# Kernel tuning notes

Measured on AMD Instinct MI355X. Metric: run time of the kernel, lower is better.

Reference implementation:

```python
import jax, jax.numpy as jnp
import numpy as np

EPS = 1e-3  # matches torch module eps
NUM_FEATURES = 64


def setup_inputs() -> dict:
    key = jax.random.key(0)
    X = jax.random.normal(key, (128, NUM_FEATURES, 56, 56), dtype=jnp.float32)
    return {"X": X}


def reference(X):
    # Training-mode decorrelated batch norm (ZCA whitening via eigendecomposition).
    N, C = X.shape[0], X.shape[1]
    # [N, C, H, W] -> [C, N*H*W]
    x = jnp.reshape(jnp.swapaxes(X, 0, 1), (C, -1))
    m = x.shape[1]
    mean = jnp.mean(x, axis=-1, keepdims=True)
    xc = x - mean
    # sigma = eps*I + (1/m) * xc @ xc^T   (C x C, SPD)
    sigma = EPS * jnp.eye(C, dtype=X.dtype) + (xc @ xc.T) / m
    # SVD of an SPD matrix == eigendecomposition; use symmetric eigh.
    eig, u = jnp.linalg.eigh(sigma)
    # wm = u @ diag(eig^-1/2) @ u^T  (inverse matrix square root)
    wm = (u * jax.lax.rsqrt(eig)) @ u.T
    xn = wm @ xc  # whiten
    # [C, N*H*W] -> [N, C, H, W]
    Xn = jnp.swapaxes(jnp.reshape(xn, (C, N) + X.shape[2:]), 0, 1)
    return Xn
```

## Files before the change

kernel.cpp:

```cpp
#include <hip/hip_runtime.h>
#include <stdint.h>

#define CCH   64
#define HWSZ  3136
#define NB    128
#define MCOLS 401408
#define TK    128
#define NTILES 3136
#define LDK   136
#define LDB   72
#define SLOT  4160
#define WS_TAIL 16512
#define RG    16
#define K1MAX 512
#define LDT   72
#define K3NB  1024
#define K3T   6272

typedef short bf16x8 __attribute__((ext_vector_type(8)));
typedef float f32x4  __attribute__((ext_vector_type(4)));
typedef unsigned short u16x4 __attribute__((ext_vector_type(4)));

__device__ __forceinline__ unsigned short f2bf(float f) {
    union { float f; uint32_t u; } v; v.f = f;
    uint32_t r = v.u + 0x7fffu + ((v.u >> 16) & 1u);
    return (unsigned short)(r >> 16);
}
__device__ __forceinline__ float bf2f(unsigned short h) {
    union { uint32_t u; float f; } v; v.u = ((uint32_t)h) << 16; return v.f;
}
__device__ __forceinline__ uint32_t fbits(float f) {
    union { float f; uint32_t u; } v; v.f = f; return v.u;
}
__device__ __forceinline__ float bcast(uint32_t u) {
    union { uint32_t u; float f; } v; v.u = u; return v.f;
}

__global__ __launch_bounds__(256) void k1_gram(const float* __restrict__ X,
                                               float* __restrict__ part,
                                               int nb) {
    __shared__ __align__(16) unsigned short tile[CCH * LDK];
    const int tid = threadIdx.x;
    const int w = tid >> 6, l = tid & 63;

    f32x4 acc[4];
    #pragma unroll
    for (int b = 0; b < 4; ++b) acc[b] = (f32x4){0.f, 0.f, 0.f, 0.f};
    float sacc[16];
    #pragma unroll
    for (int i = 0; i < 16; ++i) sacc[i] = 0.f;

    float2 xv[16];

    uint32_t t = blockIdx.x;
    {
        const uint32_t s = t * TK + 2u * (uint32_t)l;
        const uint32_t n = s / HWSZ;
        const uint32_t hw = s - n * HWSZ;
        const size_t base = (size_t)n * (CCH * HWSZ) + hw + (size_t)w * HWSZ;
        #pragma unroll
        for (int i = 0; i < 16; ++i)
            xv[i] = *(const float2*)(X + base + (size_t)i * (4u * HWSZ));
    }

    for (;;) {
        __syncthreads();
        #pragma unroll
        for (int i = 0; i < 16; ++i) {
            sacc[i] += xv[i].x + xv[i].y;
            const int c = 4 * i + w;
            *(uint32_t*)&tile[c * LDK + 2 * l] =
                (uint32_t)f2bf(xv[i].x) | ((uint32_t)f2bf(xv[i].y) << 16);
        }
        __syncthreads();

        const uint32_t tn = t + (uint32_t)nb;
        const bool more = tn < NTILES;
        if (more) {
            const uint32_t s = tn * TK + 2u * (uint32_t)l;
            const uint32_t n = s / HWSZ;
            const uint32_t hw = s - n * HWSZ;
            const size_t base = (size_t)n * (CCH * HWSZ) + hw + (size_t)w * HWSZ;
            #pragma unroll
            for (int i = 0; i < 16; ++i)
                xv[i] = *(const float2*)(X + base + (size_t)i * (4u * HWSZ));
        }

        #pragma unroll
        for (int k0 = 0; k0 < TK; k0 += 32) {
            const int koff = k0 + ((l >> 4) << 3);
            const bf16x8 fa = *(const bf16x8*)&tile[(16 * w + (l & 15)) * LDK + koff];
            #pragma unroll
            for (int bj = 0; bj < 4; ++bj) {
                const bf16x8 fb = *(const bf16x8*)&tile[(16 * bj + (l & 15)) * LDK + koff];
                acc[bj] = __builtin_amdgcn_mfma_f32_16x16x32_bf16(fa, fb, acc[bj], 0, 0, 0);
            }
        }

        if (!more) break;
        t = tn;
    }

    float* pg = part + (size_t)blockIdx.x * SLOT;
    #pragma unroll
    for (int bj = 0; bj < 4; ++bj) {
        #pragma unroll
        for (int r = 0; r < 4; ++r) {
            const int row = 16 * w + ((l >> 4) << 2) + r;
            const int col = 16 * bj + (l & 15);
            pg[row * 64 + col] = acc[bj][r];
        }
    }
    #pragma unroll
    for (int i = 0; i < 16; ++i) {
        float v = sacc[i];
        #pragma unroll
        for (int m = 32; m > 0; m >>= 1) v += __shfl_xor(v, m, 64);
        if (l == 0) pg[4096 + 4 * i + w] = v;
    }
}

__global__ __launch_bounds__(256) void k1b1_reduce(const float* __restrict__ part,
                                                   float* __restrict__ part2,
                                                   int nb) {
    const int bx = blockIdx.x;
    const int g = bx / 17;
    const int e = (bx - g * 17) * 256 + threadIdx.x;
    if (e >= SLOT) return;
    float a0 = 0.f, a1 = 0.f, a2 = 0.f, a3 = 0.f;
    int b = g;
    for (; b + 3 * RG < nb; b += 4 * RG) {
        a0 += part[(size_t)b * SLOT + e];
        a1 += part[(size_t)(b + RG) * SLOT + e];
        a2 += part[(size_t)(b + 2 * RG) * SLOT + e];
        a3 += part[(size_t)(b + 3 * RG) * SLOT + e];
    }
    for (; b < nb; b += RG) a0 += part[(size_t)b * SLOT + e];
    part2[(size_t)g * SLOT + e] = (a0 + a1) + (a2 + a3);
}

__device__ __forceinline__ bf16x8 ldfrag_h(const unsigned short* H, int rowbase, int k0, int l) {
    const int row = rowbase + (l & 15);
    const int koff = k0 + ((l >> 4) << 3);
    return *(const bf16x8*)&H[row * LDB + koff];
}
__device__ __forceinline__ bf16x8 ldfrag_lo(const float* F, bf16x8 hi, int rowbase, int k0, int l) {
    const int row = rowbase + (l & 15);
    const int koff = k0 + ((l >> 4) << 3);
    const float* p = F + row * 64 + koff;
    bf16x8 lo;
    #pragma unroll
    for (int j = 0; j < 8; ++j)
        lo[j] = (short)f2bf(p[j] - bf2f((unsigned short)hi[j]));
    return lo;
}

__device__ void mm_plain(const unsigned short* Lh, const unsigned short* Rh,
                         unsigned short* DH, float* DF, int tid) {
    const int w = tid >> 6, l = tid & 63;
    f32x4 acc[4];
    #pragma unroll
    for (int b = 0; b < 4; ++b) acc[b] = (f32x4){0.f, 0.f, 0.f, 0.f};
    #pragma unroll
    for (int k0 = 0; k0 < 64; k0 += 32) {
        const bf16x8 la = ldfrag_h(Lh, 16 * w, k0, l);
        #pragma unroll
        for (int b = 0; b < 4; ++b) {
            const bf16x8 rb = ldfrag_h(Rh, 16 * b, k0, l);
            acc[b] = __builtin_amdgcn_mfma_f32_16x16x32_bf16(la, rb, acc[b], 0, 0, 0);
        }
    }
    __syncthreads();
    #pragma unroll
    for (int b = 0; b < 4; ++b) {
        #pragma unroll
        for (int r = 0; r < 4; ++r) {
            const int row = 16 * w + ((l >> 4) << 2) + r;
            const int col = 16 * b + (l & 15);
            const float v = acc[b][r];
            if (DH) DH[row * LDB + col] = f2bf(v);
            if (DF) DF[row * 64 + col] = v;
        }
    }
    __syncthreads();
}

__device__ void mm_split(const unsigned short* Lh, const float* Lf,
                         const unsigned short* Rh, const float* Rf,
                         unsigned short* DH, float* DF, int tid) {
    const int w = tid >> 6, l = tid & 63;
    f32x4 acc[4];
    #pragma unroll
    for (int b = 0; b < 4; ++b) acc[b] = (f32x4){0.f, 0.f, 0.f, 0.f};
    #pragma unroll
    for (int k0 = 0; k0 < 64; k0 += 32) {
        const bf16x8 lah = ldfrag_h(Lh, 16 * w, k0, l);
        const bf16x8 lal = ldfrag_lo(Lf, lah, 16 * w, k0, l);
        #pragma unroll
        for (int b = 0; b < 4; ++b) {
            const bf16x8 rbh = ldfrag_h(Rh, 16 * b, k0, l);
            const bf16x8 rbl = ldfrag_lo(Rf, rbh, 16 * b, k0, l);
            acc[b] = __builtin_amdgcn_mfma_f32_16x16x32_bf16(lah, rbh, acc[b], 0, 0, 0);
            acc[b] = __builtin_amdgcn_mfma_f32_16x16x32_bf16(lah, rbl, acc[b], 0, 0, 0);
            acc[b] = __builtin_amdgcn_mfma_f32_16x16x32_bf16(lal, rbh, acc[b], 0, 0, 0);
        }
    }
    __syncthreads();
    #pragma unroll
    for (int b = 0; b < 4; ++b) {
        #pragma unroll
        for (int r = 0; r < 4; ++r) {
            const int row = 16 * w + ((l >> 4) << 2) + r;
            const int col = 16 * b + (l & 15);
            const float v = acc[b][r];
            if (DH) DH[row * LDB + col] = f2bf(v);
            if (DF) DF[row * 64 + col] = v;
        }
    }
    __syncthreads();
}

__global__ __launch_bounds__(256) void k2_ns(const float* __restrict__ part2,
                                             float* __restrict__ ws) {
    float* bvec = ws + 8256;
    float* Ag = ws + 8320;
    unsigned short* wmh = (unsigned short*)(ws + 12416);
    unsigned short* wml = (unsigned short*)(ws + 14464);

    __shared__ float Zf[4096];
    __shared__ float Sf[4096];
    __shared__ __align__(16) unsigned short Ah[64 * LDB];
    __shared__ __align__(16) unsigned short ZhA[64 * LDB];
    __shared__ __align__(16) unsigned short Bh[64 * LDB];
    __shared__ float mu[64];
    __shared__ float sred[1];

    const int tid = threadIdx.x;
    const float invm = 1.0f / (float)MCOLS;

    if (tid < 64) {
        float a = 0.f;
        #pragma unroll
        for (int b = 0; b < RG; ++b) a += part2[(size_t)b * SLOT + 4096 + tid];
        mu[tid] = a * invm;
    }
    __syncthreads();

    #pragma unroll
    for (int j = 0; j < 16; ++j) {
        const int e = tid * 16 + j;
        const int i = e >> 6, c = e & 63;
        float a0 = 0.f, a1 = 0.f, a2 = 0.f, a3 = 0.f;
        #pragma unroll
        for (int b = 0; b < RG; b += 4) {
            a0 += part2[(size_t)(b + 0) * SLOT + e];
            a1 += part2[(size_t)(b + 1) * SLOT + e];
            a2 += part2[(size_t)(b + 2) * SLOT + e];
            a3 += part2[(size_t)(b + 3) * SLOT + e];
        }
        const float g = (a0 + a1) + (a2 + a3);
        Sf[e] = g * invm - mu[i] * mu[c] + ((i == c) ? 1e-3f : 0.0f);
    }
    __syncthreads();

    if (tid < 64) {
        float rs = 0.f;
        #pragma unroll
        for (int j = 0; j < 64; ++j) {
            const int c = (j + tid) & 63;
            rs += fabsf(Sf[tid * 64 + c]);
        }
        #pragma unroll
        for (int m = 32; m > 0; m >>= 1) rs = fmaxf(rs, __shfl_xor(rs, m, 64));
        if (tid == 0) sred[0] = rs;
    }
    __syncthreads();
    const float s = sred[0];
    const float invs = 1.0f / s;

    #pragma unroll
    for (int j = 0; j < 16; ++j) {
        const int e = tid * 16 + j;
        const int i = e >> 6, c = e & 63;
        const float a = Sf[e] * invs;
        Ag[e] = a;
        Ah[i * LDB + c] = f2bf(a);
        const float z = (i == c) ? 1.0f : 0.0f;
        Zf[e] = z;
        ZhA[i * LDB + c] = f2bf(z);
    }
    __syncthreads();

    for (int itn = 0; itn < 4; ++itn) {
        mm_plain(ZhA, ZhA, Bh, nullptr, tid);
        mm_plain(Ah, Bh, Bh, nullptr, tid);
        mm_plain(ZhA, Bh, nullptr, Sf, tid);
        #pragma unroll
        for (int j = 0; j < 16; ++j) {
            const int e = tid * 16 + j;
            const int i = e >> 6, c = e & 63;
            const float z = 1.5f * Zf[e] - 0.5f * Sf[e];
            Zf[e] = z;
            ZhA[i * LDB + c] = f2bf(z);
        }
        __syncthreads();
    }

    mm_split(ZhA, Zf, ZhA, Zf, Bh, Sf, tid);
    mm_split(Ah, Ag, Bh, Sf, Bh, Sf, tid);
    mm_split(ZhA, Zf, Bh, Sf, nullptr, Sf, tid);

    const float wsq = 1.0f / sqrtf(s);
    #pragma unroll
    for (int j = 0; j < 16; ++j) {
        const int e = tid * 16 + j;
        const float z = 1.5f * Zf[e] - 0.5f * Sf[e];
        Zf[e] = z;
        const float wv = z * wsq;
        const unsigned short h = f2bf(wv);
        wmh[e] = h;
        wml[e] = f2bf(wv - bf2f(h));
    }
    __syncthreads();

    if (tid < 64) {
        float acc = 0.f;
        #pragma unroll
        for (int j = 0; j < 64; ++j) {
            const int c = (j + tid) & 63;
            acc += Zf[tid * 64 + c] * mu[c];
        }
        bvec[tid] = acc * wsq;
    }
}

__global__ __launch_bounds__(256) void k3_whiten(const float* __restrict__ X,
                                                 const float* __restrict__ ws,
                                                 float* __restrict__ out) {
    __shared__ __align__(16) unsigned short xh[64 * LDT];
    __shared__ __align__(16) unsigned short xl[64 * LDT];
    const int tid = threadIdx.x;
    const int w = tid >> 6, l = tid & 63;
    const int lm = l & 15;
    const int koffL = (l >> 4) << 3;

    const unsigned short* __restrict__ wmh = (const unsigned short*)(ws + 12416);
    const unsigned short* __restrict__ wml = (const unsigned short*)(ws + 14464);
    const float* __restrict__ bvec = ws + 8256;

    bf16x8 fbh[2][4], fbl[2][4];
    #pragma unroll
    for (int kk = 0; kk < 2; ++kk) {
        #pragma unroll
        for (int cb = 0; cb < 4; ++cb) {
            const int c = cb * 16 + lm;
            fbh[kk][cb] = *(const bf16x8*)&wmh[c * 64 + kk * 32 + koffL];
            fbl[kk][cb] = *(const bf16x8*)&wml[c * 64 + kk * 32 + koffL];
        }
    }
    float bv[4];
    #pragma unroll
    for (int cb = 0; cb < 4; ++cb) bv[cb] = bvec[cb * 16 + lm];

    float xv[16];
    uint32_t g = blockIdx.x;
    size_t base;
    {
        const uint32_t n = g / 49u;
        const uint32_t hw0 = (g - n * 49u) * 64u;
        base = (size_t)n * (CCH * HWSZ) + hw0;
        #pragma unroll
        for (int u = 0; u < 16; ++u)
            xv[u] = X[base + (size_t)(w * 16 + u) * HWSZ + l];
    }

    const int frow = (16 * w + lm) * LDT;
    const int p0 = 16 * w + ((l >> 4) << 2);

    for (;;) {
        __syncthreads();
        #pragma unroll
        for (int uu = 0; uu < 4; ++uu) {
            const int j0 = uu * 4;
            const uint32_t a0 = fbits(xv[j0 + 0]);
            const uint32_t a1 = fbits(xv[j0 + 1]);
            const uint32_t a2 = fbits(xv[j0 + 2]);
            const uint32_t a3 = fbits(xv[j0 + 3]);
            uint2 hv, lv;
            hv.x = __builtin_amdgcn_perm(a1, a0, 0x07060302u);
            hv.y = __builtin_amdgcn_perm(a3, a2, 0x07060302u);
            const float r0 = xv[j0 + 0] - bcast(a0 & 0xFFFF0000u);
            const float r1 = xv[j0 + 1] - bcast(a1 & 0xFFFF0000u);
            const float r2 = xv[j0 + 2] - bcast(a2 & 0xFFFF0000u);
            const float r3 = xv[j0 + 3] - bcast(a3 & 0xFFFF0000u);
            lv.x = __builtin_amdgcn_perm(fbits(r1), fbits(r0), 0x07060302u);
            lv.y = __builtin_amdgcn_perm(fbits(r3), fbits(r2), 0x07060302u);
            const int c0 = w * 16 + uu * 4;
            *(uint2*)&xh[l * LDT + c0] = hv;
            *(uint2*)&xl[l * LDT + c0] = lv;
        }
        __syncthreads();

        const uint32_t gn = g + K3NB;
        const bool more = gn < K3T;
        size_t basen = 0;
        if (more) {
            const uint32_t n = gn / 49u;
            const uint32_t hw0 = (gn - n * 49u) * 64u;
            basen = (size_t)n * (CCH * HWSZ) + hw0;
            #pragma unroll
            for (int u = 0; u < 16; ++u)
                xv[u] = X[basen + (size_t)(w * 16 + u) * HWSZ + l];
        }

        f32x4 acc[4];
        #pragma unroll
        for (int b = 0; b < 4; ++b) acc[b] = (f32x4){0.f, 0.f, 0.f, 0.f};
        #pragma unroll
        for (int kk = 0; kk < 2; ++kk) {
            const bf16x8 fah = *(const bf16x8*)&xh[frow + kk * 32 + koffL];
            const bf16x8 fal = *(const bf16x8*)&xl[frow + kk * 32 + koffL];
            #pragma unroll
            for (int cb = 0; cb < 4; ++cb) {
                acc[cb] = __builtin_amdgcn_mfma_f32_16x16x32_bf16(fah, fbh[kk][cb], acc[cb], 0, 0, 0);
                acc[cb] = __builtin_amdgcn_mfma_f32_16x16x32_bf16(fah, fbl[kk][cb], acc[cb], 0, 0, 0);
                acc[cb] = __builtin_amdgcn_mfma_f32_16x16x32_bf16(fal, fbh[kk][cb], acc[cb], 0, 0, 0);
            }
        }

        #pragma unroll
        for (int cb = 0; cb < 4; ++cb) {
            const int c = cb * 16 + lm;
            f32x4 v;
            v[0] = acc[cb][0] - bv[cb];
            v[1] = acc[cb][1] - bv[cb];
            v[2] = acc[cb][2] - bv[cb];
            v[3] = acc[cb][3] - bv[cb];
            *(f32x4*)&out[base + (size_t)c * HWSZ + p0] = v;
        }

        if (!more) break;
        g = gn;
        base = basen;
    }
}

extern "C" void kernel_launch(void* const* d_in, const int* in_sizes, int n_in,
                              void* d_out, int out_size, void* d_ws, size_t ws_size,
                              hipStream_t stream) {
    (void)in_sizes; (void)n_in; (void)out_size;
    const float* X = (const float*)d_in[0];
    float* out = (float*)d_out;
    float* ws = (float*)d_ws;

    long avail = (long)(ws_size / sizeof(float)) - WS_TAIL - (long)RG * SLOT;
    int nb = (int)(avail / SLOT);
    if (nb > K1MAX) nb = K1MAX;
    if (nb < 1) nb = 1;

    float* part = ws + WS_TAIL;
    float* part2 = part + (size_t)nb * SLOT;

    k1_gram<<<nb, 256, 0, stream>>>(X, part, nb);
    k1b1_reduce<<<17 * RG, 256, 0, stream>>>(part, part2, nb);
    k2_ns<<<1, 256, 0, stream>>>(part2, ws);
    k3_whiten<<<K3NB, 256, 0, stream>>>(X, ws, out);
}
```

Baseline: 242.3 us.

## Fuse Newton-Schulz whitening-matrix solve redundantly into every whitening block

The single-block Newton-Schulz kernel is removed. Its work, computing the inverse square root of the 64x64 covariance, is now recomputed redundantly inside each of 512 whitening blocks, which read a fully reduced Gram matrix produced by a new small reduction kernel. The aim is to remove the serial one-block kernel and its launch gap, and to overlap the first X tile load with the matrix iteration. In exchange every block repeats the small matrix solve, uses a large LDS arena that limits occupancy, and the grid is halved.

```diff
diff --git a/kernel.cpp b/kernel.cpp
--- a/kernel.cpp
+++ b/kernel.cpp
@@ -14,7 +14,7 @@
 #define RG    16
 #define K1MAX 512
 #define LDT   72
-#define K3NB  1024
+#define GRID3 512
 #define K3T   6272
 
 typedef short bf16x8 __attribute__((ext_vector_type(8)));
@@ -139,6 +139,21 @@
     part2[(size_t)g * SLOT + e] = (a0 + a1) + (a2 + a3);
 }
 
+__global__ __launch_bounds__(256) void k1b2_reduce(const float* __restrict__ part2,
+                                                   float* __restrict__ out) {
+    const int e = blockIdx.x * 256 + threadIdx.x;
+    if (e >= SLOT) return;
+    float a0 = 0.f, a1 = 0.f, a2 = 0.f, a3 = 0.f;
+    #pragma unroll
+    for (int b = 0; b < RG; b += 4) {
+        a0 += part2[(size_t)b * SLOT + e];
+        a1 += part2[(size_t)(b + 1) * SLOT + e];
+        a2 += part2[(size_t)(b + 2) * SLOT + e];
+        a3 += part2[(size_t)(b + 3) * SLOT + e];
+    }
+    out[e] = (a0 + a1) + (a2 + a3);
+}
+
 __device__ __forceinline__ bf16x8 ldfrag_h(const unsigned short* H, int rowbase, int k0, int l) {
     const int row = rowbase + (l & 15);
     const int koff = k0 + ((l >> 4) << 3);
@@ -220,147 +235,28 @@
     __syncthreads();
 }
 
-__global__ __launch_bounds__(256) void k2_ns(const float* __restrict__ part2,
-                                             float* __restrict__ ws) {
-    float* bvec = ws + 8256;
-    float* Ag = ws + 8320;
-    unsigned short* wmh = (unsigned short*)(ws + 12416);
-    unsigned short* wml = (unsigned short*)(ws + 14464);
-
-    __shared__ float Zf[4096];
-    __shared__ float Sf[4096];
-    __shared__ __align__(16) unsigned short Ah[64 * LDB];
-    __shared__ __align__(16) unsigned short ZhA[64 * LDB];
-    __shared__ __align__(16) unsigned short Bh[64 * LDB];
-    __shared__ float mu[64];
-    __shared__ float sred[1];
-
-    const int tid = threadIdx.x;
-    const float invm = 1.0f / (float)MCOLS;
-
-    if (tid < 64) {
-        float a = 0.f;
-        #pragma unroll
-        for (int b = 0; b < RG; ++b) a += part2[(size_t)b * SLOT + 4096 + tid];
-        mu[tid] = a * invm;
-    }
-    __syncthreads();
-
-    #pragma unroll
-    for (int j = 0; j < 16; ++j) {
-        const int e = tid * 16 + j;
-        const int i = e >> 6, c = e & 63;
-        float a0 = 0.f, a1 = 0.f, a2 = 0.f, a3 = 0.f;
-        #pragma unroll
-        for (int b = 0; b < RG; b += 4) {
-            a0 += part2[(size_t)(b + 0) * SLOT + e];
-            a1 += part2[(size_t)(b + 1) * SLOT + e];
-            a2 += part2[(size_t)(b + 2) * SLOT + e];
-            a3 += part2[(size_t)(b + 3) * SLOT + e];
-        }
-        const float g = (a0 + a1) + (a2 + a3);
-        Sf[e] = g * invm - mu[i] * mu[c] + ((i == c) ? 1e-3f : 0.0f);
-    }
-    __syncthreads();
-
-    if (tid < 64) {
-        float rs = 0.f;
-        #pragma unroll
-        for (int j = 0; j < 64; ++j) {
-            const int c = (j + tid) & 63;
-            rs += fabsf(Sf[tid * 64 + c]);
-        }
-        #pragma unroll
-        for (int m = 32; m > 0; m >>= 1) rs = fmaxf(rs, __shfl_xor(rs, m, 64));
-        if (tid == 0) sred[0] = rs;
-    }
-    __syncthreads();
-    const float s = sred[0];
-    const float invs = 1.0f / s;
-
-    #pragma unroll
-    for (int j = 0; j < 16; ++j) {
-        const int e = tid * 16 + j;
-        const int i = e >> 6, c = e & 63;
-        const float a = Sf[e] * invs;
-        Ag[e] = a;
-        Ah[i * LDB + c] = f2bf(a);
-        const float z = (i == c) ? 1.0f : 0.0f;
-        Zf[e] = z;
-        ZhA[i * LDB + c] = f2bf(z);
-    }
-    __syncthreads();
-
-    for (int itn = 0; itn < 4; ++itn) {
-        mm_plain(ZhA, ZhA, Bh, nullptr, tid);
-        mm_plain(Ah, Bh, Bh, nullptr, tid);
-        mm_plain(ZhA, Bh, nullptr, Sf, tid);
-        #pragma unroll
-        for (int j = 0; j < 16; ++j) {
-            const int e = tid * 16 + j;
-            const int i = e >> 6, c = e & 63;
-            const float z = 1.5f * Zf[e] - 0.5f * Sf[e];
-            Zf[e] = z;
-            ZhA[i * LDB + c] = f2bf(z);
-        }
-        __syncthreads();
-    }
-
-    mm_split(ZhA, Zf, ZhA, Zf, Bh, Sf, tid);
-    mm_split(Ah, Ag, Bh, Sf, Bh, Sf, tid);
-    mm_split(ZhA, Zf, Bh, Sf, nullptr, Sf, tid);
-
-    const float wsq = 1.0f / sqrtf(s);
-    #pragma unroll
-    for (int j = 0; j < 16; ++j) {
-        const int e = tid * 16 + j;
-        const float z = 1.5f * Zf[e] - 0.5f * Sf[e];
-        Zf[e] = z;
-        const float wv = z * wsq;
-        const unsigned short h = f2bf(wv);
-        wmh[e] = h;
-        wml[e] = f2bf(wv - bf2f(h));
-    }
-    __syncthreads();
-
-    if (tid < 64) {
-        float acc = 0.f;
-        #pragma unroll
-        for (int j = 0; j < 64; ++j) {
-            const int c = (j + tid) & 63;
-            acc += Zf[tid * 64 + c] * mu[c];
-        }
-        bvec[tid] = acc * wsq;
-    }
-}
-
-__global__ __launch_bounds__(256) void k3_whiten(const float* __restrict__ X,
-                                                 const float* __restrict__ ws,
-                                                 float* __restrict__ out) {
-    __shared__ __align__(16) unsigned short xh[64 * LDT];
-    __shared__ __align__(16) unsigned short xl[64 * LDT];
+__global__ __launch_bounds__(256, 2) void k3_fused(const float* __restrict__ X,
+                                                   const float* __restrict__ ws,
+                                                   float* __restrict__ out) {
+    __shared__ __align__(16) char arena[77328];
+    float* Zf = (float*)arena;
+    float* Sf = (float*)(arena + 16384);
+    float* Af = (float*)(arena + 32768);
+    unsigned short* Ah  = (unsigned short*)(arena + 49152);
+    unsigned short* ZhA = (unsigned short*)(arena + 58368);
+    unsigned short* Bh  = (unsigned short*)(arena + 67584);
+    float* mu   = (float*)(arena + 76800);
+    float* bvf  = (float*)(arena + 77056);
+    float* sred = (float*)(arena + 77312);
+    unsigned short* xh = (unsigned short*)arena;
+    unsigned short* xl = (unsigned short*)(arena + 9216);
+    unsigned short* wmhd = (unsigned short*)(arena + 49152);
+    unsigned short* wmld = (unsigned short*)(arena + 58368);
+
     const int tid = threadIdx.x;
     const int w = tid >> 6, l = tid & 63;
     const int lm = l & 15;
     const int koffL = (l >> 4) << 3;
-
-    const unsigned short* __restrict__ wmh = (const unsigned short*)(ws + 12416);
-    const unsigned short* __restrict__ wml = (const unsigned short*)(ws + 14464);
-    const float* __restrict__ bvec = ws + 8256;
-
-    bf16x8 fbh[2][4], fbl[2][4];
-    #pragma unroll
-    for (int kk = 0; kk < 2; ++kk) {
-        #pragma unroll
-        for (int cb = 0; cb < 4; ++cb) {
-            const int c = cb * 16 + lm;
-            fbh[kk][cb] = *(const bf16x8*)&wmh[c * 64 + kk * 32 + koffL];
-            fbl[kk][cb] = *(const bf16x8*)&wml[c * 64 + kk * 32 + koffL];
-        }
-    }
-    float bv[4];
-    #pragma unroll
-    for (int cb = 0; cb < 4; ++cb) bv[cb] = bvec[cb * 16 + lm];
 
     float xv[16];
     uint32_t g = blockIdx.x;
@@ -373,6 +269,104 @@
         for (int u = 0; u < 16; ++u)
             xv[u] = X[base + (size_t)(w * 16 + u) * HWSZ + l];
     }
+
+    const float invm = 1.0f / (float)MCOLS;
+
+    if (tid < 64) mu[tid] = ws[4096 + tid] * invm;
+    __syncthreads();
+
+    #pragma unroll
+    for (int j = 0; j < 16; ++j) {
+        const int e = tid * 16 + j;
+        const int i = e >> 6, c = e & 63;
+        Sf[e] = ws[e] * invm - mu[i] * mu[c] + ((i == c) ? 1e-3f : 0.0f);
+    }
+    __syncthreads();
+
+    if (tid < 64) {
+        float rs = 0.f;
+        #pragma unroll
+        for (int j = 0; j < 64; ++j) {
+            const int c = (j + tid) & 63;
+            rs += fabsf(Sf[tid * 64 + c]);
+        }
+        #pragma unroll
+        for (int m = 32; m > 0; m >>= 1) rs = fmaxf(rs, __shfl_xor(rs, m, 64));
+        if (tid == 0) sred[0] = rs;
+    }
+    __syncthreads();
+    const float s = sred[0];
+    const float invs = 1.0f / s;
+
+    #pragma unroll
+    for (int j = 0; j < 16; ++j) {
+        const int e = tid * 16 + j;
+        const int i = e >> 6, c = e & 63;
+        const float a = Sf[e] * invs;
+        Af[e] = a;
+        Ah[i * LDB + c] = f2bf(a);
+        const float z = (i == c) ? 1.0f : 0.0f;
+        Zf[e] = z;
+        ZhA[i * LDB + c] = f2bf(z);
+    }
+    __syncthreads();
+
+    for (int itn = 0; itn < 4; ++itn) {
+        mm_plain(ZhA, ZhA, Bh, nullptr, tid);
+        mm_plain(Ah, Bh, Bh, nullptr, tid);
+        mm_plain(ZhA, Bh, nullptr, Sf, tid);
+        #pragma unroll
+        for (int j = 0; j < 16; ++j) {
+            const int e = tid * 16 + j;
+            const int i = e >> 6, c = e & 63;
+            const float z = 1.5f * Zf[e] - 0.5f * Sf[e];
+            Zf[e] = z;
+            ZhA[i * LDB + c] = f2bf(z);
+        }
+        __syncthreads();
+    }
+
+    mm_split(ZhA, Zf, ZhA, Zf, Bh, Sf, tid);
+    mm_split(Ah, Af, Bh, Sf, Bh, Sf, tid);
+    mm_split(ZhA, Zf, Bh, Sf, nullptr, Sf, tid);
+
+    const float wsq = 1.0f / sqrtf(s);
+    #pragma unroll
+    for (int j = 0; j < 16; ++j) {
+        const int e = tid * 16 + j;
+        const float z = 1.5f * Zf[e] - 0.5f * Sf[e];
+        Zf[e] = z;
+        const float wv = z * wsq;
+        const unsigned short h = f2bf(wv);
+        wmhd[e] = h;
+        wmld[e] = f2bf(wv - bf2f(h));
+    }
+    __syncthreads();
+
+    if (tid < 64) {
+        float acc = 0.f;
+        #pragma unroll
+        for (int j = 0; j < 64; ++j) {
+            const int c = (j + tid) & 63;
+            acc += Zf[tid * 64 + c] * mu[c];
+        }
+        bvf[tid] = acc * wsq;
+    }
+    __syncthreads();
+
+    bf16x8 fbh[2][4], fbl[2][4];
+    #pragma unroll
+    for (int kk = 0; kk < 2; ++kk) {
+        #pragma unroll
+        for (int cb = 0; cb < 4; ++cb) {
+            const int c = cb * 16 + lm;
+            fbh[kk][cb] = *(const bf16x8*)&wmhd[c * 64 + kk * 32 + koffL];
+            fbl[kk][cb] = *(const bf16x8*)&wmld[c * 64 + kk * 32 + koffL];
+        }
+    }
+    float bv[4];
+    #pragma unroll
+    for (int cb = 0; cb < 4; ++cb) bv[cb] = bvf[cb * 16 + lm];
 
     const int frow = (16 * w + lm) * LDT;
     const int p0 = 16 * w + ((l >> 4) << 2);
@@ -401,7 +395,7 @@
         }
         __syncthreads();
 
-        const uint32_t gn = g + K3NB;
+        const uint32_t gn = g + (uint32_t)GRID3;
         const bool more = gn < K3T;
         size_t basen = 0;
         if (more) {
@@ -463,6 +457,6 @@
 
     k1_gram<<<nb, 256, 0, stream>>>(X, part, nb);
     k1b1_reduce<<<17 * RG, 256, 0, stream>>>(part, part2, nb);
-    k2_ns<<<1, 256, 0, stream>>>(part2, ws);
-    k3_whiten<<<K3NB, 256, 0, stream>>>(X, ws, out);
-}
+    k1b2_reduce<<<17, 256, 0, stream>>>(part2, ws);
+    k3_fused<<<GRID3, 256, 0, stream>>>(X, ws, out);
+}
```

Measured after the change: 254.0 us. +4.8%, slower.
